# Optimization experiments

Hardware: AMD Instinct MI355X
Metric: run time of the kernel (lower is better)

Reference implementation:

```python
import jax, jax.numpy as jnp
import numpy as np

B, H, W, DIM, WS, NH, HID = 16, 64, 64, 256, 8, 8, 1024
SHIFT = WS // 2
N = WS * WS  # tokens per window


def _rel_pos_index(ws):
    coords = np.stack(np.meshgrid(np.arange(ws), np.arange(ws), indexing='ij')).reshape(2, -1)
    rel = (coords[:, :, None] - coords[:, None, :]).transpose(1, 2, 0)  # [n,n,2]
    rel[..., 0] += ws - 1
    rel[..., 1] += ws - 1
    rel[..., 0] *= 2 * ws - 1
    return rel.sum(-1)  # [n,n] ints in [0, (2ws-1)^2)


def _attn_mask(h, w, ws, ss):
    img = np.zeros((h, w), np.float32)
    cnt = 0
    sl = (slice(0, -ws), slice(-ws, -ss), slice(-ss, None))
    for hs in sl:
        for wsl in sl:
            img[hs, wsl] = cnt
            cnt += 1
    mw = img.reshape(h // ws, ws, w // ws, ws).transpose(0, 2, 1, 3).reshape(-1, ws * ws)
    d = mw[:, None, :] - mw[:, :, None]  # unsqueeze(1) - unsqueeze(2)
    return np.where(d != 0, np.float32(-100.0), np.float32(0.0))  # [nW,n,n]


RPI = jnp.asarray(_rel_pos_index(WS).reshape(-1))          # [n*n] int
MASK = jnp.asarray(_attn_mask(H, W, WS, SHIFT))            # [nW,n,n]


def ln(x, g, b, eps):
    m = x.mean(-1, keepdims=True)
    v = x.var(-1, keepdims=True)
    return (x - m) / jnp.sqrt(v + eps) * g + b


def win_part(x, ws):
    b, h, w, c = x.shape
    x = x.reshape(b, h // ws, ws, w // ws, ws, c).transpose(0, 1, 3, 2, 4, 5)
    return x.reshape(-1, ws * ws, c)  # [b*nW, n, c]


def win_rev(win, ws, h, w):
    c = win.shape[-1]
    b = win.shape[0] // ((h // ws) * (w // ws))
    x = win.reshape(b, h // ws, w // ws, ws, ws, c).transpose(0, 1, 3, 2, 4, 5)
    return x.reshape(b, h, w, c)


def attention(xw, qkv_w, qkv_b, rpb, out_w, out_b, mask):
    Bw, n, c = xw.shape
    dh = c // NH
    scale = dh ** -0.5
    qkv = (xw @ qkv_w + qkv_b).reshape(Bw, n, 3, NH, dh).transpose(2, 0, 3, 1, 4)
    q, k, v = qkv[0], qkv[1], qkv[2]                       # [Bw,NH,n,dh]
    dots = jnp.einsum('bhid,bhjd->bhij', q, k) * scale
    bias = rpb[RPI].reshape(n, n, NH).transpose(2, 0, 1)   # [NH,n,n]
    attn = dots + bias[None]
    if mask is not None:
        nW = mask.shape[0]
        attn = attn.reshape(Bw // nW, nW, NH, n, n) + mask[None, :, None]
        attn = attn.reshape(Bw, NH, n, n)
    attn = jax.nn.softmax(attn, axis=-1)
    out = jnp.einsum('bhij,bhjd->bhid', attn, v)
    out = out.transpose(0, 2, 1, 3).reshape(Bw, n, c)
    return out @ out_w + out_b


def block(x, shifted, mask, n1g, n1b, qkv_w, qkv_b, rpb, out_w, out_b,
          n2g, n2b, lng, lnb, w1, b1, w2, b2):
    b, l, c = x.shape
    shortcut = x
    x = ln(x, n1g, n1b, 1e-5).reshape(b, H, W, c)
    if shifted:
        x = jnp.roll(x, (-SHIFT, -SHIFT), (1, 2))
    xw = win_part(x, WS)
    xw = attention(xw, qkv_w, qkv_b, rpb, out_w, out_b, mask)
    x = win_rev(xw, WS, H, W)
    if shifted:
        x = jnp.roll(x, (SHIFT, SHIFT), (1, 2))
    x = shortcut + x.reshape(b, l, c)
    # FeedForward contains its own LayerNorm(eps=1e-6) after norm2 (faithful to source)
    h = ln(x, n2g, n2b, 1e-5)
    h = ln(h, lng, lnb, 1e-6)
    h = jax.nn.gelu(h @ w1 + b1, approximate=False) @ w2 + b2
    return x + h


def forward(x, *p):
    x = block(x, False, None, *p[0:15])
    x = block(x, True, MASK, *p[15:30])
    return x


def setup_inputs() -> dict:
    key = jax.random.key(0)
    ks = iter(jax.random.split(key, 16))
    s = 0.02
    d = {'x': jax.random.normal(next(ks), (B, H * W, DIM), jnp.float32)}
    for i in (0, 1):
        p = f'b{i}_'
        d[p + 'n1g'] = jnp.ones((DIM,), jnp.float32)
        d[p + 'n1b'] = jnp.zeros((DIM,), jnp.float32)
        d[p + 'qkv_w'] = jax.random.normal(next(ks), (DIM, 3 * DIM), jnp.float32) * s
        d[p + 'qkv_b'] = jnp.zeros((3 * DIM,), jnp.float32)
        d[p + 'rpb'] = jax.random.normal(next(ks), ((2 * WS - 1) ** 2, NH), jnp.float32) * s
        d[p + 'out_w'] = jax.random.normal(next(ks), (DIM, DIM), jnp.float32) * s
        d[p + 'out_b'] = jnp.zeros((DIM,), jnp.float32)
        d[p + 'n2g'] = jnp.ones((DIM,), jnp.float32)
        d[p + 'n2b'] = jnp.zeros((DIM,), jnp.float32)
        d[p + 'lng'] = jnp.ones((DIM,), jnp.float32)
        d[p + 'lnb'] = jnp.zeros((DIM,), jnp.float32)
        d[p + 'w1'] = jax.random.normal(next(ks), (DIM, HID), jnp.float32) * s
        d[p + 'b1'] = jnp.zeros((HID,), jnp.float32)
        d[p + 'w2'] = jax.random.normal(next(ks), (HID, DIM), jnp.float32) * s
        d[p + 'b2'] = jnp.zeros((DIM,), jnp.float32)
    return d


def reference(x,
              b0_n1g, b0_n1b, b0_qkv_w, b0_qkv_b, b0_rpb, b0_out_w, b0_out_b,
              b0_n2g, b0_n2b, b0_lng, b0_lnb, b0_w1, b0_b1, b0_w2, b0_b2,
              b1_n1g, b1_n1b, b1_qkv_w, b1_qkv_b, b1_rpb, b1_out_w, b1_out_b,
              b1_n2g, b1_n2b, b1_lng, b1_lnb, b1_w1, b1_b1, b1_w2, b1_b2):
    return forward(x,
                   b0_n1g, b0_n1b, b0_qkv_w, b0_qkv_b, b0_rpb, b0_out_w, b0_out_b,
                   b0_n2g, b0_n2b, b0_lng, b0_lnb, b0_w1, b0_b1, b0_w2, b0_b2,
                   b1_n1g, b1_n1b, b1_qkv_w, b1_qkv_b, b1_rpb, b1_out_w, b1_out_b,
                   b1_n2g, b1_n2b, b1_lng, b1_lnb, b1_w1, b1_b1, b1_w2, b1_b2)
```

## Files before the change

### kernel.cpp

```cpp
#include <hip/hip_runtime.h>

typedef unsigned short u16;
typedef __attribute__((ext_vector_type(8))) short bf16x8;
typedef __attribute__((ext_vector_type(8))) unsigned short u16x8;
typedef __attribute__((ext_vector_type(4))) unsigned short u16x4;
typedef __attribute__((ext_vector_type(4))) float f32x4;

__device__ inline float b2f(u16 u) {
    union { unsigned u32; float f; } x; x.u32 = ((unsigned)u) << 16; return x.f;
}
__device__ inline u16 f2b(float f) {
    union { float f; unsigned u; } x; x.f = f;
    unsigned r = x.u + 0x7fffu + ((x.u >> 16) & 1u);
    return (u16)(r >> 16);
}

__device__ inline float fast_gelu(float v) {
    float x = fabsf(v) * 0.70710678118654752f;
    float t = __builtin_amdgcn_rcpf(1.0f + 0.3275911f * x);
    float e = __expf(-x * x);
    float poly = ((((1.061405429f * t - 1.453152027f) * t + 1.421413741f) * t
                   - 0.284496736f) * t + 0.254829592f) * t;
    float erfv = 1.0f - poly * e;
    float w = copysignf(erfv, v);
    return 0.5f * v * (1.0f + w);
}

#define GLOAD_LDS16(g, l) \
    __builtin_amdgcn_global_load_lds((const __attribute__((address_space(1))) void*)(const void*)(g), \
                                     (__attribute__((address_space(3))) void*)(void*)(l), 16, 0, 0)
#define FENCE() asm volatile("" ::: "memory")

__global__ __launch_bounds__(256)
void ln_win_kernel(const float* __restrict__ x, const float* __restrict__ g,
                   const float* __restrict__ b, u16* __restrict__ xw, int shift)
{
    int wid = blockIdx.x * 4 + (threadIdx.x >> 6);
    int lane = threadIdx.x & 63;
    int win = wid >> 6, tok = wid & 63;
    int bb = win >> 6, wib = win & 63;
    int h = (((wib >> 3) << 3) + (tok >> 3) + shift) & 63;
    int w = (((wib & 7) << 3) + (tok & 7) + shift) & 63;
    size_t src = ((size_t)bb * 4096 + h * 64 + w) * 256;
    float4 v = ((const float4*)(x + src))[lane];
    float s = v.x + v.y + v.z + v.w;
    float s2 = v.x*v.x + v.y*v.y + v.z*v.z + v.w*v.w;
    for (int k = 32; k > 0; k >>= 1) { s += __shfl_xor(s, k); s2 += __shfl_xor(s2, k); }
    float mean = s * (1.f/256.f);
    float var  = s2 * (1.f/256.f) - mean*mean;
    float rs = rsqrtf(var + 1e-5f);
    int c = lane * 4;
    u16x4 o;
    o[0] = f2b((v.x - mean) * rs * g[c+0] + b[c+0]);
    o[1] = f2b((v.y - mean) * rs * g[c+1] + b[c+1]);
    o[2] = f2b((v.z - mean) * rs * g[c+2] + b[c+2]);
    o[3] = f2b((v.w - mean) * rs * g[c+3] + b[c+3]);
    *(u16x4*)(xw + (size_t)wid * 256 + c) = o;
}

__global__ __launch_bounds__(256)
void ln2_kernel(const float* __restrict__ xin,
                const float* __restrict__ g1, const float* __restrict__ b1,
                const float* __restrict__ g2, const float* __restrict__ b2,
                u16* __restrict__ out)
{
    int wid = blockIdx.x * 4 + (threadIdx.x >> 6);
    int lane = threadIdx.x & 63;
    float4 v = ((const float4*)(xin + (size_t)wid * 256))[lane];
    float s = v.x + v.y + v.z + v.w;
    float s2 = v.x*v.x + v.y*v.y + v.z*v.z + v.w*v.w;
    for (int k = 32; k > 0; k >>= 1) { s += __shfl_xor(s, k); s2 += __shfl_xor(s2, k); }
    float mean = s * (1.f/256.f);
    float var  = s2 * (1.f/256.f) - mean*mean;
    float rs = rsqrtf(var + 1e-5f);
    int c = lane * 4;
    float y0 = (v.x - mean) * rs * g1[c+0] + b1[c+0];
    float y1 = (v.y - mean) * rs * g1[c+1] + b1[c+1];
    float y2 = (v.z - mean) * rs * g1[c+2] + b1[c+2];
    float y3 = (v.w - mean) * rs * g1[c+3] + b1[c+3];
    float t = y0 + y1 + y2 + y3;
    float t2 = y0*y0 + y1*y1 + y2*y2 + y3*y3;
    for (int k = 32; k > 0; k >>= 1) { t += __shfl_xor(t, k); t2 += __shfl_xor(t2, k); }
    float m2 = t * (1.f/256.f);
    float v2 = t2 * (1.f/256.f) - m2*m2;
    float rs2 = rsqrtf(v2 + 1e-6f);
    u16x4 o;
    o[0] = f2b((y0 - m2) * rs2 * g2[c+0] + b2[c+0]);
    o[1] = f2b((y1 - m2) * rs2 * g2[c+1] + b2[c+1]);
    o[2] = f2b((y2 - m2) * rs2 * g2[c+2] + b2[c+2]);
    o[3] = f2b((y3 - m2) * rs2 * g2[c+3] + b2[c+3]);
    *(u16x4*)(out + (size_t)wid * 256 + c) = o;
}

__global__ __launch_bounds__(256)
void transpose_w(const float* __restrict__ W, u16* __restrict__ Wt, int K, int N)
{
    __shared__ float t[32][33];
    int nb = blockIdx.x * 32, kb = blockIdx.y * 32;
    int tx = threadIdx.x & 31, ty = threadIdx.x >> 5;
    #pragma unroll
    for (int r = 0; r < 32; r += 8)
        t[ty + r][tx] = W[(size_t)(kb + ty + r) * N + nb + tx];
    __syncthreads();
    #pragma unroll
    for (int r = 0; r < 32; r += 8)
        Wt[(size_t)(nb + ty + r) * K + kb + tx] = f2b(t[tx][ty + r]);
}

__global__ __launch_bounds__(256)
void build_bias(const float* __restrict__ rpb, float* __restrict__ bmT)
{
    int idx = blockIdx.x * 256 + threadIdx.x;
    int q = idx & 63, k = (idx >> 6) & 63, h = (idx >> 12) & 7, cls = idx >> 15;
    int qh = q >> 3, qw = q & 7, kh = k >> 3, kw = k & 7;
    float v = rpb[((qh - kh + 7) * 15 + (qw - kw + 7)) * 8 + h];
    int ch = cls >> 1, cw = cls & 1;
    int rq = (ch ? (qh < 4 ? 1 : 2) : 0) * 3 + (cw ? (qw < 4 ? 1 : 2) : 0);
    int rk = (ch ? (kh < 4 ? 1 : 2) : 0) * 3 + (cw ? (kw < 4 ? 1 : 2) : 0);
    if (rq != rk) v -= 100.f;
    bmT[idx] = v * 1.4426950408889634f;
}

template<int EPI>
__global__ __launch_bounds__(256)
void gemm_k4(const u16* __restrict__ A, const u16* __restrict__ Bt,
             const float* __restrict__ bias, void* __restrict__ out,
             const float* __restrict__ resid, int M, int N, int K, int shift)
{
    __shared__ u16 As[4][128][32];
    __shared__ u16 Bs[4][128][32];
    const int tid = threadIdx.x, lane = tid & 63, wv = tid >> 6;
    const int g = lane >> 4, r = lane & 15;
    const int wr = wv >> 1, wc = wv & 1;
    const int nwg = gridDim.x * gridDim.y;
    const int lid = blockIdx.y * gridDim.x + blockIdx.x;
    const int qq = nwg >> 3, r8 = nwg & 7;
    const int xcd = lid & 7, pos = lid >> 3;
    const int nid = (xcd < r8 ? xcd * (qq + 1) : r8 * (qq + 1) + (xcd - r8) * qq) + pos;
    const int bm = nid / gridDim.x, bn = nid % gridDim.x;

    f32x4 acc[4][4] = {};
    const int arow = wv * 16 + (lane >> 2);
    const int scol = (((lane & 3) ^ ((lane >> 2) & 3) ^ ((lane >> 4) & 1)) * 8);
    const u16* gA = A + (size_t)(bm * 128 + arow) * K + scol;
    const u16* gB = Bt + (size_t)(bn * 128 + arow) * K + scol;
    const int nk = K >> 5;
    const int rc = (g ^ (r & 3) ^ ((r >> 2) & 1)) * 8;

#define STAGE(t) do { \
        u16* a_ = &As[(t) & 3][0][0]; u16* b_ = &Bs[(t) & 3][0][0]; \
        GLOAD_LDS16(gA + (size_t)(t) * 32,                    a_ + wv * 512); \
        GLOAD_LDS16(gA + (size_t)(t) * 32 + (size_t)64 * K,   a_ + 2048 + wv * 512); \
        GLOAD_LDS16(gB + (size_t)(t) * 32,                    b_ + wv * 512); \
        GLOAD_LDS16(gB + (size_t)(t) * 32 + (size_t)64 * K,   b_ + 2048 + wv * 512); \
    } while (0)

    STAGE(0);
    STAGE(1);
    for (int kt = 0; kt < nk; ++kt) {
        const int cur = kt & 3;
        if (kt + 2 < nk) {
            STAGE(kt + 2);
            asm volatile("s_waitcnt vmcnt(8)" ::: "memory");
        } else if (kt + 1 < nk) {
            asm volatile("s_waitcnt vmcnt(4)" ::: "memory");
        } else {
            asm volatile("s_waitcnt vmcnt(0)" ::: "memory");
        }
        __builtin_amdgcn_s_barrier();
        FENCE();
        bf16x8 af[4], bf[4];
        #pragma unroll
        for (int i = 0; i < 4; ++i)
            af[i] = *(const bf16x8*)(&As[cur][wr * 64 + i * 16 + r][rc]);
        #pragma unroll
        for (int j = 0; j < 4; ++j)
            bf[j] = *(const bf16x8*)(&Bs[cur][wc * 64 + j * 16 + r][rc]);
        __builtin_amdgcn_s_setprio(1);
        #pragma unroll
        for (int j = 0; j < 4; ++j)
            #pragma unroll
            for (int i = 0; i < 4; ++i)
                acc[j][i] = __builtin_amdgcn_mfma_f32_16x16x32_bf16(bf[j], af[i], acc[j][i], 0, 0, 0);
        __builtin_amdgcn_s_setprio(0);
        asm volatile("s_waitcnt lgkmcnt(0)" ::: "memory");
        __builtin_amdgcn_sched_barrier(0);
    }
#undef STAGE

    #pragma unroll
    for (int i = 0; i < 4; ++i) {
        const int row = bm * 128 + wr * 64 + i * 16 + r;
        size_t orow;
        if (EPI == 2) {
            int win = row >> 6, tok = row & 63;
            int bb = win >> 6, wib = win & 63;
            int h = (((wib >> 3) << 3) + (tok >> 3) + shift) & 63;
            int w = (((wib & 7) << 3) + (tok & 7) + shift) & 63;
            orow = (size_t)bb * 4096 + h * 64 + w;
        } else {
            orow = (size_t)row;
        }
        #pragma unroll
        for (int j = 0; j < 4; ++j) {
            const int colb = bn * 128 + wc * 64 + j * 16 + g * 4;
            const float4 bv = *(const float4*)(bias + colb);
            if (EPI == 0) {
                u16x4 o;
                o[0] = f2b(acc[j][i][0] + bv.x);
                o[1] = f2b(acc[j][i][1] + bv.y);
                o[2] = f2b(acc[j][i][2] + bv.z);
                o[3] = f2b(acc[j][i][3] + bv.w);
                *(u16x4*)((u16*)out + (size_t)row * N + colb) = o;
            } else if (EPI == 1) {
                u16x4 o;
                o[0] = f2b(fast_gelu(acc[j][i][0] + bv.x));
                o[1] = f2b(fast_gelu(acc[j][i][1] + bv.y));
                o[2] = f2b(fast_gelu(acc[j][i][2] + bv.z));
                o[3] = f2b(fast_gelu(acc[j][i][3] + bv.w));
                *(u16x4*)((u16*)out + (size_t)row * N + colb) = o;
            } else {
                const float4 rv = *(const float4*)(resid + orow * N + colb);
                float4 o;
                o.x = rv.x + acc[j][i][0] + bv.x;
                o.y = rv.y + acc[j][i][1] + bv.y;
                o.z = rv.z + acc[j][i][2] + bv.z;
                o.w = rv.w + acc[j][i][3] + bv.w;
                *(float4*)((float*)out + orow * N + colb) = o;
            }
        }
    }
}

template<int SHIFTED>
__global__ __launch_bounds__(256)
void attn_mfma(const u16* __restrict__ qkv, const float* __restrict__ bmT,
               u16* __restrict__ out)
{
    __shared__ u16 pbuf[4][64 * 72];
    __shared__ u16 vbuf[4][32 * 72];
    const int tid = threadIdx.x, lane = tid & 63, wv = tid >> 6;
    const int g = lane >> 4, r = lane & 15;
    const int win = blockIdx.x;
    u16* P  = pbuf[wv];
    u16* Vt = vbuf[wv];
    const u16* base = qkv + (size_t)win * 64 * 768;
    int cls = 0;
    if (SHIFTED) {
        int wib = win & 63;
        cls = (((wib >> 3) == 7) ? 2 : 0) + (((wib & 7) == 7) ? 1 : 0);
    }
    const float sc = 0.17677669529663687f * 1.4426950408889634f;

    for (int hh = 0; hh < 2; ++hh) {
        const int h = wv * 2 + hh;
        const float* bmh = bmT + ((size_t)cls * 8 + h) * 4096;
        bf16x8 kf[4], qf[4];
        #pragma unroll
        for (int i = 0; i < 4; ++i) {
            kf[i] = *(const bf16x8*)(base + (size_t)(i * 16 + r) * 768 + 256 + h * 32 + g * 8);
            qf[i] = *(const bf16x8*)(base + (size_t)(i * 16 + r) * 768 +       h * 32 + g * 8);
        }
        #pragma unroll
        for (int d0 = 0; d0 < 32; d0 += 8) {
            u16x8 vv = *(const u16x8*)(base + (size_t)lane * 768 + 512 + h * 32 + d0);
            #pragma unroll
            for (int e = 0; e < 8; ++e) Vt[(d0 + e) * 72 + lane] = vv[e];
        }
        f32x4 acc[4][4] = {};
        #pragma unroll
        for (int i = 0; i < 4; ++i)
            #pragma unroll
            for (int j = 0; j < 4; ++j)
                acc[i][j] = __builtin_amdgcn_mfma_f32_16x16x32_bf16(kf[i], qf[j], acc[i][j], 0, 0, 0);
        #pragma unroll
        for (int i = 0; i < 4; ++i) {
            const int kb = (i * 16 + g * 4) * 64;
            #pragma unroll
            for (int j = 0; j < 4; ++j) {
                const int qq = j * 16 + r;
                #pragma unroll
                for (int rr = 0; rr < 4; ++rr)
                    acc[i][j][rr] = acc[i][j][rr] * sc + bmh[kb + rr * 64 + qq];
            }
        }
        float inv_[4];
        #pragma unroll
        for (int j = 0; j < 4; ++j) {
            float m = acc[0][j][0];
            #pragma unroll
            for (int i = 0; i < 4; ++i)
                #pragma unroll
                for (int rr = 0; rr < 4; ++rr) m = fmaxf(m, acc[i][j][rr]);
            m = fmaxf(m, __shfl_xor(m, 16));
            m = fmaxf(m, __shfl_xor(m, 32));
            float s = 0.f;
            #pragma unroll
            for (int i = 0; i < 4; ++i)
                #pragma unroll
                for (int rr = 0; rr < 4; ++rr) {
                    float p = exp2f(acc[i][j][rr] - m);
                    acc[i][j][rr] = p; s += p;
                }
            s += __shfl_xor(s, 16);
            s += __shfl_xor(s, 32);
            inv_[j] = 1.f / s;
        }
        #pragma unroll
        for (int j = 0; j < 4; ++j) {
            const float iv = inv_[j];
            #pragma unroll
            for (int i = 0; i < 4; ++i) {
                u16x4 w;
                #pragma unroll
                for (int rr = 0; rr < 4; ++rr) w[rr] = f2b(acc[i][j][rr] * iv);
                *(u16x4*)(P + (j * 16 + r) * 72 + i * 16 + g * 4) = w;
            }
        }
        f32x4 o[2][4] = {};
        #pragma unroll
        for (int ks = 0; ks < 2; ++ks) {
            bf16x8 pa[4], vb[2];
            #pragma unroll
            for (int i = 0; i < 4; ++i)
                pa[i] = *(const bf16x8*)(P + (i * 16 + r) * 72 + ks * 32 + g * 8);
            #pragma unroll
            for (int j = 0; j < 2; ++j)
                vb[j] = *(const bf16x8*)(Vt + (j * 16 + r) * 72 + ks * 32 + g * 8);
            #pragma unroll
            for (int j = 0; j < 2; ++j)
                #pragma unroll
                for (int i = 0; i < 4; ++i)
                    o[j][i] = __builtin_amdgcn_mfma_f32_16x16x32_bf16(vb[j], pa[i], o[j][i], 0, 0, 0);
        }
        u16* op = out + (size_t)win * 64 * 256 + h * 32;
        #pragma unroll
        for (int i = 0; i < 4; ++i) {
            const int qrow = i * 16 + r;
            #pragma unroll
            for (int j = 0; j < 2; ++j) {
                u16x4 w;
                #pragma unroll
                for (int rr = 0; rr < 4; ++rr) w[rr] = f2b(o[j][i][rr]);
                *(u16x4*)(op + (size_t)qrow * 256 + j * 16 + g * 4) = w;
            }
        }
    }
}

extern "C" void kernel_launch(void* const* d_in, const int* in_sizes, int n_in,
                              void* d_out, int out_size, void* d_ws, size_t ws_size,
                              hipStream_t stream)
{
    (void)in_sizes; (void)n_in; (void)out_size; (void)ws_size;
    const float* x = (const float*)d_in[0];
    char* ws = (char*)d_ws;
    size_t off = 0;
    auto alloc = [&](size_t bytes) { void* p = ws + off; off += (bytes + 255) & ~(size_t)255; return p; };

    u16 *wtq[2], *wto[2], *wt1[2], *wt2[2];
    float* bmT[2];
    for (int i = 0; i < 2; ++i) {
        wtq[i] = (u16*)alloc((size_t)768 * 256 * 2);
        wto[i] = (u16*)alloc((size_t)256 * 256 * 2);
        wt1[i] = (u16*)alloc((size_t)1024 * 256 * 2);
        wt2[i] = (u16*)alloc((size_t)256 * 1024 * 2);
        bmT[i] = (float*)alloc((size_t)4 * 8 * 64 * 64 * 4);
    }
    u16*  xw  = (u16*)alloc((size_t)65536 * 256 * 2);
    u16*  big = (u16*)alloc((size_t)65536 * 1024 * 2);
    float* x1 = (float*)alloc((size_t)65536 * 256 * 4);
    float* outp = (float*)d_out;

    for (int blk = 0; blk < 2; ++blk) {
        const float* const* P = (const float* const*)(d_in + 1 + blk * 15);
        transpose_w<<<dim3(768 / 32, 256 / 32), 256, 0, stream>>>(P[2], wtq[blk], 256, 768);
        transpose_w<<<dim3(256 / 32, 256 / 32), 256, 0, stream>>>(P[5], wto[blk], 256, 256);
        transpose_w<<<dim3(1024 / 32, 256 / 32), 256, 0, stream>>>(P[11], wt1[blk], 256, 1024);
        transpose_w<<<dim3(256 / 32, 1024 / 32), 256, 0, stream>>>(P[13], wt2[blk], 1024, 256);
        build_bias<<<512, 256, 0, stream>>>(P[4], bmT[blk]);
    }

    for (int blk = 0; blk < 2; ++blk) {
        const float* const* P = (const float* const*)(d_in + 1 + blk * 15);
        const int sh = blk ? 4 : 0;
        const float* xin = blk ? outp : x;

        ln_win_kernel<<<16384, 256, 0, stream>>>(xin, P[0], P[1], xw, sh);
        gemm_k4<0><<<dim3(6, 512), 256, 0, stream>>>(xw, wtq[blk], P[3], big, nullptr, 65536, 768, 256, 0);
        if (blk) attn_mfma<1><<<1024, 256, 0, stream>>>(big, bmT[blk], xw);
        else     attn_mfma<0><<<1024, 256, 0, stream>>>(big, bmT[blk], xw);
        gemm_k4<2><<<dim3(2, 512), 256, 0, stream>>>(xw, wto[blk], P[6], x1, xin, 65536, 256, 256, sh);
        ln2_kernel<<<16384, 256, 0, stream>>>(x1, P[7], P[8], P[9], P[10], xw);
        gemm_k4<1><<<dim3(8, 512), 256, 0, stream>>>(xw, wt1[blk], P[12], big, nullptr, 65536, 1024, 256, 0);
        gemm_k4<3><<<dim3(2, 512), 256, 0, stream>>>(big, wt2[blk], P[14], outp, x1, 65536, 256, 1024, 0);
    }
}
```

Measured before the change: 723.1 us.

## Add register-resident-A GEMM for K=256 projections, streaming B tiles through LDS

Adds a new GEMM kernel for the K=256 GEMMs (QKV, output projection, FC1). Each 512-thread block holds a 256-row A slab in registers and loops over all N columns, double-buffering 64-column B tiles through LDS. A is read from global memory only once instead of once per column tile, and the FC2 GEMM keeps the old kernel, now specialised to its residual epilogue. The risks are heavy register pressure from the resident A fragments and a fixed grid of 256 blocks, which may limit occupancy and the overlap of loads with compute.

```diff
diff --git a/kernel.cpp b/kernel.cpp
--- a/kernel.cpp
+++ b/kernel.cpp
@@ -122,6 +122,115 @@
 }
 
 template<int EPI>
+__global__ __launch_bounds__(512)
+void gemm_areg(const u16* __restrict__ A, const u16* __restrict__ Bt,
+               const float* __restrict__ bias, void* __restrict__ out,
+               const float* __restrict__ resid, int N, int shift)
+{
+    constexpr int K = 256;
+    __shared__ u16 Bs[2][8][64][32];
+    const int tid = threadIdx.x, lane = tid & 63, wv = tid >> 6;
+    const int g = lane >> 4, r = lane & 15;
+    const int bid = blockIdx.x;
+    const int bm = (bid & 7) * 32 + (bid >> 3);
+    const int row0 = bm * 256 + wv * 32;
+
+    bf16x8 af[2][8];
+    #pragma unroll
+    for (int rf = 0; rf < 2; ++rf)
+        #pragma unroll
+        for (int ks = 0; ks < 8; ++ks)
+            af[rf][ks] = *(const bf16x8*)(A + (size_t)(row0 + rf * 16 + r) * K + ks * 32 + g * 8);
+
+    const int NB = N >> 6;
+#define STAGE(bn_, buf_) do { \
+        _Pragma("unroll") \
+        for (int it = 0; it < 4; ++it) { \
+            const int L8 = it * 512 + tid; \
+            const int c4 = L8 & 3, rowp = (L8 >> 2) & 63, kc = L8 >> 8; \
+            const u16* src = Bt + (size_t)((bn_) * 64 + rowp) * K + kc * 32 + c4 * 8; \
+            GLOAD_LDS16(src, &Bs[buf_][0][0][0] + (size_t)(it * 512 + wv * 64) * 8); \
+        } \
+    } while (0)
+
+    STAGE(0, 0);
+    int cur = 0;
+    for (int bn = 0; bn < NB; ++bn) {
+        if (bn + 1 < NB) {
+            STAGE(bn + 1, cur ^ 1);
+            asm volatile("s_waitcnt vmcnt(4)" ::: "memory");
+        } else {
+            asm volatile("s_waitcnt vmcnt(0)" ::: "memory");
+        }
+        __builtin_amdgcn_s_barrier();
+        FENCE();
+        f32x4 acc[4][2] = {};
+        #pragma unroll
+        for (int ks = 0; ks < 8; ++ks) {
+            bf16x8 bf[4];
+            #pragma unroll
+            for (int cf = 0; cf < 4; ++cf)
+                bf[cf] = *(const bf16x8*)(&Bs[cur][ks][cf * 16 + r][g * 8]);
+            __builtin_amdgcn_s_setprio(1);
+            #pragma unroll
+            for (int cf = 0; cf < 4; ++cf)
+                #pragma unroll
+                for (int rf = 0; rf < 2; ++rf)
+                    acc[cf][rf] = __builtin_amdgcn_mfma_f32_16x16x32_bf16(bf[cf], af[rf][ks], acc[cf][rf], 0, 0, 0);
+            __builtin_amdgcn_s_setprio(0);
+        }
+        asm volatile("s_waitcnt lgkmcnt(0)" ::: "memory");
+        __builtin_amdgcn_sched_barrier(0);
+        __builtin_amdgcn_s_barrier();
+        FENCE();
+        #pragma unroll
+        for (int rf = 0; rf < 2; ++rf) {
+            const int row = row0 + rf * 16 + r;
+            size_t orow;
+            if (EPI == 2) {
+                int win = row >> 6, tok = row & 63;
+                int bb = win >> 6, wib = win & 63;
+                int h = (((wib >> 3) << 3) + (tok >> 3) + shift) & 63;
+                int w = (((wib & 7) << 3) + (tok & 7) + shift) & 63;
+                orow = (size_t)bb * 4096 + h * 64 + w;
+            } else {
+                orow = (size_t)row;
+            }
+            #pragma unroll
+            for (int cf = 0; cf < 4; ++cf) {
+                const int colb = bn * 64 + cf * 16 + g * 4;
+                const float4 bv = *(const float4*)(bias + colb);
+                if (EPI == 0) {
+                    u16x4 o;
+                    o[0] = f2b(acc[cf][rf][0] + bv.x);
+                    o[1] = f2b(acc[cf][rf][1] + bv.y);
+                    o[2] = f2b(acc[cf][rf][2] + bv.z);
+                    o[3] = f2b(acc[cf][rf][3] + bv.w);
+                    *(u16x4*)((u16*)out + (size_t)row * N + colb) = o;
+                } else if (EPI == 1) {
+                    u16x4 o;
+                    o[0] = f2b(fast_gelu(acc[cf][rf][0] + bv.x));
+                    o[1] = f2b(fast_gelu(acc[cf][rf][1] + bv.y));
+                    o[2] = f2b(fast_gelu(acc[cf][rf][2] + bv.z));
+                    o[3] = f2b(fast_gelu(acc[cf][rf][3] + bv.w));
+                    *(u16x4*)((u16*)out + (size_t)row * N + colb) = o;
+                } else {
+                    const float4 rv = *(const float4*)(resid + orow * N + colb);
+                    float4 o;
+                    o.x = rv.x + acc[cf][rf][0] + bv.x;
+                    o.y = rv.y + acc[cf][rf][1] + bv.y;
+                    o.z = rv.z + acc[cf][rf][2] + bv.z;
+                    o.w = rv.w + acc[cf][rf][3] + bv.w;
+                    *(float4*)((float*)out + orow * N + colb) = o;
+                }
+            }
+        }
+        cur ^= 1;
+    }
+#undef STAGE
+}
+
+template<int EPI>
 __global__ __launch_bounds__(256)
 void gemm_k4(const u16* __restrict__ A, const u16* __restrict__ Bt,
              const float* __restrict__ bias, void* __restrict__ out,
@@ -138,7 +247,6 @@
     const int xcd = lid & 7, pos = lid >> 3;
     const int nid = (xcd < r8 ? xcd * (qq + 1) : r8 * (qq + 1) + (xcd - r8) * qq) + pos;
     const int bm = nid / gridDim.x, bn = nid % gridDim.x;
-
     f32x4 acc[4][4] = {};
     const int arow = wv * 16 + (lane >> 2);
     const int scol = (((lane & 3) ^ ((lane >> 2) & 3) ^ ((lane >> 4) & 1)) * 8);
@@ -191,43 +299,17 @@
     #pragma unroll
     for (int i = 0; i < 4; ++i) {
         const int row = bm * 128 + wr * 64 + i * 16 + r;
-        size_t orow;
-        if (EPI == 2) {
-            int win = row >> 6, tok = row & 63;
-            int bb = win >> 6, wib = win & 63;
-            int h = (((wib >> 3) << 3) + (tok >> 3) + shift) & 63;
-            int w = (((wib & 7) << 3) + (tok & 7) + shift) & 63;
-            orow = (size_t)bb * 4096 + h * 64 + w;
-        } else {
-            orow = (size_t)row;
-        }
         #pragma unroll
         for (int j = 0; j < 4; ++j) {
             const int colb = bn * 128 + wc * 64 + j * 16 + g * 4;
             const float4 bv = *(const float4*)(bias + colb);
-            if (EPI == 0) {
-                u16x4 o;
-                o[0] = f2b(acc[j][i][0] + bv.x);
-                o[1] = f2b(acc[j][i][1] + bv.y);
-                o[2] = f2b(acc[j][i][2] + bv.z);
-                o[3] = f2b(acc[j][i][3] + bv.w);
-                *(u16x4*)((u16*)out + (size_t)row * N + colb) = o;
-            } else if (EPI == 1) {
-                u16x4 o;
-                o[0] = f2b(fast_gelu(acc[j][i][0] + bv.x));
-                o[1] = f2b(fast_gelu(acc[j][i][1] + bv.y));
-                o[2] = f2b(fast_gelu(acc[j][i][2] + bv.z));
-                o[3] = f2b(fast_gelu(acc[j][i][3] + bv.w));
-                *(u16x4*)((u16*)out + (size_t)row * N + colb) = o;
-            } else {
-                const float4 rv = *(const float4*)(resid + orow * N + colb);
-                float4 o;
-                o.x = rv.x + acc[j][i][0] + bv.x;
-                o.y = rv.y + acc[j][i][1] + bv.y;
-                o.z = rv.z + acc[j][i][2] + bv.z;
-                o.w = rv.w + acc[j][i][3] + bv.w;
-                *(float4*)((float*)out + orow * N + colb) = o;
-            }
+            const float4 rv = *(const float4*)(resid + (size_t)row * N + colb);
+            float4 o;
+            o.x = rv.x + acc[j][i][0] + bv.x;
+            o.y = rv.y + acc[j][i][1] + bv.y;
+            o.z = rv.z + acc[j][i][2] + bv.z;
+            o.w = rv.w + acc[j][i][3] + bv.w;
+            *(float4*)((float*)out + (size_t)row * N + colb) = o;
         }
     }
 }
@@ -387,12 +469,12 @@
         const float* xin = blk ? outp : x;
 
         ln_win_kernel<<<16384, 256, 0, stream>>>(xin, P[0], P[1], xw, sh);
-        gemm_k4<0><<<dim3(6, 512), 256, 0, stream>>>(xw, wtq[blk], P[3], big, nullptr, 65536, 768, 256, 0);
+        gemm_areg<0><<<256, 512, 0, stream>>>(xw, wtq[blk], P[3], big, nullptr, 768, 0);
         if (blk) attn_mfma<1><<<1024, 256, 0, stream>>>(big, bmT[blk], xw);
         else     attn_mfma<0><<<1024, 256, 0, stream>>>(big, bmT[blk], xw);
-        gemm_k4<2><<<dim3(2, 512), 256, 0, stream>>>(xw, wto[blk], P[6], x1, xin, 65536, 256, 256, sh);
+        gemm_areg<2><<<256, 512, 0, stream>>>(xw, wto[blk], P[6], x1, xin, 256, sh);
         ln2_kernel<<<16384, 256, 0, stream>>>(x1, P[7], P[8], P[9], P[10], xw);
-        gemm_k4<1><<<dim3(8, 512), 256, 0, stream>>>(xw, wt1[blk], P[12], big, nullptr, 65536, 1024, 256, 0);
+        gemm_areg<1><<<256, 512, 0, stream>>>(xw, wt1[blk], P[12], big, nullptr, 1024, 0);
         gemm_k4<3><<<dim3(2, 512), 256, 0, stream>>>(big, wt2[blk], P[14], outp, x1, 65536, 256, 1024, 0);
     }
 }
```

Measured after the change: 796.6 us. 1.1x slower.
